# Kernel tuning notes

Hardware: AMD Instinct MI355X
Metric: run time of the kernel (lower is better)

Reference implementation:

```python
import jax, jax.numpy as jnp
import numpy as np

B, D, E = 8192, 4096, 64
TOP_K = 2
NOISE_EPSILON = 0.01


def setup_inputs() -> dict:
    key = jax.random.key(0)
    k1, k2, k3, k4 = jax.random.split(key, 4)
    return {
        "x": jax.random.normal(k1, (B, D), dtype=jnp.float32),
        # nn.Linear weights, init std=0.1, no bias; torch stores [out, in]
        "gate_w": jax.random.normal(k2, (E, D), dtype=jnp.float32) * 0.1,
        "noise_gate_w": jax.random.normal(k3, (E, D), dtype=jnp.float32) * 0.1,
        # deterministic stand-in for torch.randn_like(clean_logits)
        "noise": jax.random.normal(k4, (B, E), dtype=jnp.float32),
    }


def reference(x, gate_w, noise_gate_w, noise):
    # clean_logits = x @ W_g^T : [B, E]
    clean_logits = jnp.einsum("bd,ed->be", x, gate_w)
    # training path: noisy logits with softplus-scaled noise
    noise_logits = jnp.einsum("bd,ed->be", x, noise_gate_w)
    noisy_logits = clean_logits + noise * jax.nn.softplus(noise_logits) * NOISE_EPSILON
    # top-k over experts, softmax over the k selected logits
    top_k_logits, top_k_indices = jax.lax.top_k(noisy_logits, TOP_K)  # [B, k]
    top_k_gates = jax.nn.softmax(top_k_logits, axis=-1)
    # scatter back into dense [B, E] gates
    rows = jnp.arange(noisy_logits.shape[0])[:, None]  # [B, 1]
    gates = jnp.zeros_like(noisy_logits).at[rows, top_k_indices].set(top_k_gates)
    load = jax.nn.softmax(clean_logits, axis=-1)
    return (gates, load)
```

## Files before the change

### kernel.cpp

```cpp
#include <hip/hip_runtime.h>
#include <math.h>

#define BB 8192
#define DD 4096
#define EE 64

constexpr float NOISE_EPS = 0.01f;
constexpr int BM  = 64;
constexpr int BK  = 32;
constexpr int WRN = 128;

typedef __attribute__((ext_vector_type(8))) _Float16 f16x8;
typedef __attribute__((ext_vector_type(4))) float    f32x4;

__device__ __forceinline__ void split8(const float4& a, const float4& b,
                                       f16x8& hi, f16x8& mi) {
    float v[8] = {a.x, a.y, a.z, a.w, b.x, b.y, b.z, b.w};
    #pragma unroll
    for (int j = 0; j < 8; ++j) {
        _Float16 h = (_Float16)v[j];
        hi[j] = h;
        mi[j] = (_Float16)(v[j] - (float)h);
    }
}

__device__ __forceinline__ void gl_lds16(const void* g, void* l) {
    __builtin_amdgcn_global_load_lds(
        (const __attribute__((address_space(1))) unsigned*)g,
        (__attribute__((address_space(3))) unsigned*)l, 16, 0, 0);
}

__global__ __launch_bounds__(256) void wsplit_pack(
    const float* __restrict__ gw, const float* __restrict__ ngw,
    char* __restrict__ wpk)
{
    const int gid = blockIdx.x * 256 + threadIdx.x;
    const int r   = gid >> 9;
    const int kc  = gid & 511;
    const int k0  = kc * 8;
    const float* src = (r < EE) ? gw + (size_t)r * DD + k0
                                : ngw + (size_t)(r - EE) * DD + k0;
    float4 a = *reinterpret_cast<const float4*>(src);
    float4 b = *reinterpret_cast<const float4*>(src + 4);
    f16x8 hi, mi;
    split8(a, b, hi, mi);
    const int T    = k0 >> 5;
    const int kq   = (k0 >> 3) & 3;
    const int cb   = r >> 4;
    const int lane = kq * 16 + (r & 15);
    char* base = wpk + (size_t)T * 16384;
    *reinterpret_cast<f16x8*>(base + ((cb * 2 + 0) * 64 + lane) * 16) = hi;
    *reinterpret_cast<f16x8*>(base + ((cb * 2 + 1) * 64 + lane) * 16) = mi;
}

template <int SK>
__global__ __launch_bounds__(512, 4) void gating_main(
    const float* __restrict__ x,
    const char*  __restrict__ wpk,
    float* __restrict__ partial)
{
    constexpr int KC  = DD / SK;
    constexpr int NKS = KC / BK;

    __shared__ __align__(1024) char xbuf[2][8192];
    __shared__ __align__(1024) char wbuf[2][16384];

    const int tid  = threadIdx.x;
    const int bid  = blockIdx.x;
    const int sk   = bid & (SK - 1);
    const int row0 = (bid / SK) * BM;
    const int lane = tid & 63;
    const int wv   = tid >> 6;
    const int wmi  = wv >> 2;
    const int wni  = wv & 3;
    const int l15  = lane & 15;
    const int kq   = lane >> 4;

    const int xrow = tid >> 3;
    const int xch  = tid & 7;
    const float* xg = x + (size_t)(row0 + xrow) * DD + sk * KC
                        + ((xch ^ (xrow & 7)) << 2);
    const char* wg = wpk + (size_t)(sk * NKS) * 16384 + tid * 16;

    char* xd0 = xbuf[0] + wv * 1024;  char* xd1 = xbuf[1] + wv * 1024;
    char* wa0 = wbuf[0] + wv * 1024;  char* wa1 = wbuf[1] + wv * 1024;
    char* wb0 = wbuf[0] + 8192 + wv * 1024;  char* wb1 = wbuf[1] + 8192 + wv * 1024;

    int xoff[2][2];
    #pragma unroll
    for (int mb = 0; mb < 2; ++mb) {
        const int r = wmi * 32 + mb * 16 + l15;
        #pragma unroll
        for (int u = 0; u < 2; ++u)
            xoff[mb][u] = r * 128 + (((kq * 2 + u) ^ (r & 7)) << 4);
    }
    int boff[2][2];
    #pragma unroll
    for (int nb = 0; nb < 2; ++nb) {
        const int cb = wni * 2 + nb;
        #pragma unroll
        for (int p = 0; p < 2; ++p)
            boff[nb][p] = ((cb * 2 + p) * 64 + lane) * 16;
    }

    f32x4 acc00 = {0.f,0.f,0.f,0.f}, acc01 = {0.f,0.f,0.f,0.f};
    f32x4 acc10 = {0.f,0.f,0.f,0.f}, acc11 = {0.f,0.f,0.f,0.f};

    gl_lds16(xg,            xd0);
    gl_lds16(wg,            wa0);
    gl_lds16(wg + 8192,     wb0);
    gl_lds16(xg + BK,       xd1);
    gl_lds16(wg + 16384,    wa1);
    gl_lds16(wg + 16384 + 8192, wb1);
    asm volatile("s_waitcnt vmcnt(3)" ::: "memory");
    __builtin_amdgcn_s_barrier();

    #pragma unroll 2
    for (int t = 0; t < NKS; ++t) {
        const int c = t & 1;
        const char* xb = xbuf[c];
        const char* wb = wbuf[c];

        f16x8 ah0, am0, ah1, am1;
        {
            float4 a0 = *reinterpret_cast<const float4*>(xb + xoff[0][0]);
            float4 a1 = *reinterpret_cast<const float4*>(xb + xoff[0][1]);
            float4 a2 = *reinterpret_cast<const float4*>(xb + xoff[1][0]);
            float4 a3 = *reinterpret_cast<const float4*>(xb + xoff[1][1]);
            split8(a0, a1, ah0, am0);
            split8(a2, a3, ah1, am1);
        }
        f16x8 bh0 = *reinterpret_cast<const f16x8*>(wb + boff[0][0]);
        f16x8 bm0 = *reinterpret_cast<const f16x8*>(wb + boff[0][1]);
        f16x8 bh1 = *reinterpret_cast<const f16x8*>(wb + boff[1][0]);
        f16x8 bm1 = *reinterpret_cast<const f16x8*>(wb + boff[1][1]);

        acc00 = __builtin_amdgcn_mfma_f32_16x16x32_f16(ah0, bh0, acc00, 0, 0, 0);
        acc01 = __builtin_amdgcn_mfma_f32_16x16x32_f16(ah0, bh1, acc01, 0, 0, 0);
        acc10 = __builtin_amdgcn_mfma_f32_16x16x32_f16(ah1, bh0, acc10, 0, 0, 0);
        acc11 = __builtin_amdgcn_mfma_f32_16x16x32_f16(ah1, bh1, acc11, 0, 0, 0);
        acc00 = __builtin_amdgcn_mfma_f32_16x16x32_f16(am0, bh0, acc00, 0, 0, 0);
        acc01 = __builtin_amdgcn_mfma_f32_16x16x32_f16(am0, bh1, acc01, 0, 0, 0);
        acc10 = __builtin_amdgcn_mfma_f32_16x16x32_f16(am1, bh0, acc10, 0, 0, 0);
        acc11 = __builtin_amdgcn_mfma_f32_16x16x32_f16(am1, bh1, acc11, 0, 0, 0);
        acc00 = __builtin_amdgcn_mfma_f32_16x16x32_f16(ah0, bm0, acc00, 0, 0, 0);
        acc01 = __builtin_amdgcn_mfma_f32_16x16x32_f16(ah0, bm1, acc01, 0, 0, 0);
        acc10 = __builtin_amdgcn_mfma_f32_16x16x32_f16(ah1, bm0, acc10, 0, 0, 0);
        acc11 = __builtin_amdgcn_mfma_f32_16x16x32_f16(ah1, bm1, acc11, 0, 0, 0);

        asm volatile("s_waitcnt lgkmcnt(0)" ::: "memory");
        __builtin_amdgcn_s_barrier();

        if (t + 2 < NKS) {
            const char* wsrc = wg + (size_t)(t + 2) * 16384;
            gl_lds16(xg + (size_t)(t + 2) * BK, c ? xd1 : xd0);
            gl_lds16(wsrc,        c ? wa1 : wa0);
            gl_lds16(wsrc + 8192, c ? wb1 : wb0);
            asm volatile("s_waitcnt vmcnt(3)" ::: "memory");
        } else {
            asm volatile("s_waitcnt vmcnt(0)" ::: "memory");
        }
        __builtin_amdgcn_s_barrier();
    }

    const size_t pbase = ((size_t)sk * BB + row0) * 128;
    #pragma unroll
    for (int j = 0; j < 4; ++j) {
        const int r0 = wmi * 32 + kq * 4 + j;
        const int c0 = wni * 32 + l15;
        partial[pbase + (size_t)r0 * 128 + c0]           = acc00[j];
        partial[pbase + (size_t)r0 * 128 + c0 + 16]      = acc01[j];
        partial[pbase + (size_t)(r0 + 16) * 128 + c0]      = acc10[j];
        partial[pbase + (size_t)(r0 + 16) * 128 + c0 + 16] = acc11[j];
    }
}

template <int SK>
__global__ __launch_bounds__(512) void gating_epi(
    const float* __restrict__ partial,
    const float* __restrict__ noise,
    float* __restrict__ out)
{
    const int tid  = threadIdx.x;
    const int wv   = tid >> 6;
    const int lane = tid & 63;
    const int l15  = lane & 15;
    const int kq   = lane >> 4;
    const int grow = blockIdx.x * 32 + wv * 4 + kq;
    const int s    = l15;

    const float* pb = partial + (size_t)grow * 128 + 4 * s;
    float4 c4 = {0.f,0.f,0.f,0.f}, n4 = {0.f,0.f,0.f,0.f};
    #pragma unroll
    for (int k = 0; k < SK; ++k) {
        const float* p = pb + (size_t)k * BB * 128;
        float4 a = *reinterpret_cast<const float4*>(p);
        float4 b = *reinterpret_cast<const float4*>(p + 64);
        c4.x += a.x; c4.y += a.y; c4.z += a.z; c4.w += a.w;
        n4.x += b.x; n4.y += b.y; n4.z += b.z; n4.w += b.w;
    }

    float4 nz = *reinterpret_cast<const float4*>(noise + (size_t)grow * EE + 4 * s);

    float cc[4] = {c4.x, c4.y, c4.z, c4.w};
    float nl[4] = {n4.x, n4.y, n4.z, n4.w};
    float m1 = -3.4e38f, m2 = -3.4e38f;
    int   i1 = -1, i2 = -1;
    float cmax = -3.4e38f;
    #pragma unroll
    for (int j = 0; j < 4; ++j) {
        const int e = 4 * s + j;
        float sp  = fmaxf(nl[j], 0.0f) + log1pf(expf(-fabsf(nl[j])));
        float nzj = (j == 0) ? nz.x : (j == 1) ? nz.y : (j == 2) ? nz.z : nz.w;
        float vno = fmaf(nzj * sp, NOISE_EPS, cc[j]);
        if (vno > m1)      { m2 = m1; i2 = i1; m1 = vno; i1 = e; }
        else if (vno > m2) { m2 = vno; i2 = e; }
        cmax = fmaxf(cmax, cc[j]);
    }

    #pragma unroll
    for (int m = 1; m < 16; m <<= 1) {
        float b1 = __shfl_xor(m1, m, 16);
        int  bi1 = __shfl_xor(i1, m, 16);
        float b2 = __shfl_xor(m2, m, 16);
        int  bi2 = __shfl_xor(i2, m, 16);
        cmax = fmaxf(cmax, __shfl_xor(cmax, m, 16));

        bool bwin = (b1 > m1) || (b1 == m1 && bi1 < i1);
        float t1; int ti1; float t2; int ti2;
        if (bwin) {
            t1 = b1; ti1 = bi1;
            bool aw = (m1 > b2) || (m1 == b2 && i1 < bi2);
            t2 = aw ? m1 : b2; ti2 = aw ? i1 : bi2;
        } else {
            t1 = m1; ti1 = i1;
            bool bw = (b1 > m2) || (b1 == m2 && bi1 < i2);
            t2 = bw ? b1 : m2; ti2 = bw ? bi1 : i2;
        }
        m1 = t1; i1 = ti1; m2 = t2; i2 = ti2;
    }

    float tq = expf(m2 - m1);
    float p1 = 1.0f / (1.0f + tq);
    float p2 = tq * p1;

    float e0 = expf(cc[0] - cmax);
    float e1 = expf(cc[1] - cmax);
    float e2 = expf(cc[2] - cmax);
    float e3 = expf(cc[3] - cmax);
    float sum = e0 + e1 + e2 + e3;
    #pragma unroll
    for (int m = 1; m < 16; m <<= 1) sum += __shfl_xor(sum, m, 16);
    float inv = 1.0f / sum;

    const int eb = 4 * s;
    float4 gt;
    gt.x = (eb     == i1) ? p1 : (eb     == i2) ? p2 : 0.0f;
    gt.y = (eb + 1 == i1) ? p1 : (eb + 1 == i2) ? p2 : 0.0f;
    gt.z = (eb + 2 == i1) ? p1 : (eb + 2 == i2) ? p2 : 0.0f;
    gt.w = (eb + 3 == i1) ? p1 : (eb + 3 == i2) ? p2 : 0.0f;
    float4 ld = {e0 * inv, e1 * inv, e2 * inv, e3 * inv};

    *reinterpret_cast<float4*>(out + (size_t)grow * EE + eb) = gt;
    *reinterpret_cast<float4*>(out + (size_t)BB * EE + (size_t)grow * EE + eb) = ld;
}

extern "C" void kernel_launch(void* const* d_in, const int* in_sizes, int n_in,
                              void* d_out, int out_size, void* d_ws, size_t ws_size,
                              hipStream_t stream) {
    const float* x     = (const float*)d_in[0];
    const float* gw    = (const float*)d_in[1];
    const float* ngw   = (const float*)d_in[2];
    const float* noise = (const float*)d_in[3];
    float* out = (float*)d_out;

    char*  wpk     = (char*)d_ws;
    float* partial = (float*)(wpk + (size_t)2 * 1024 * 1024);

    const size_t MB = 1024 * 1024;

    hipLaunchKernelGGL(wsplit_pack, dim3(256), dim3(256), 0, stream, gw, ngw, wpk);

    if (ws_size >= 18 * MB) {
        hipLaunchKernelGGL(gating_main<4>, dim3((BB / BM) * 4), dim3(512), 0, stream,
                           x, wpk, partial);
        hipLaunchKernelGGL(gating_epi<4>, dim3(BB / 32), dim3(512), 0, stream,
                           partial, noise, out);
    } else if (ws_size >= 10 * MB) {
        hipLaunchKernelGGL(gating_main<2>, dim3((BB / BM) * 2), dim3(512), 0, stream,
                           x, wpk, partial);
        hipLaunchKernelGGL(gating_epi<2>, dim3(BB / 32), dim3(512), 0, stream,
                           partial, noise, out);
    } else {
        hipLaunchKernelGGL(gating_main<1>, dim3(BB / BM), dim3(512), 0, stream,
                           x, wpk, partial);
        hipLaunchKernelGGL(gating_epi<1>, dim3(BB / 32), dim3(512), 0, stream,
                           partial, noise, out);
    }
}
```

Baseline: 54.81 us.

## Deepen x prefetch to three stages and remap warps to 16x64 tiles

The main GEMM kernel now triple-buffers the x tiles while keeping double-buffered weights, so x loads are issued three steps ahead and weight loads two steps ahead. Warps are remapped from a 2x4 grid of 32x32 tiles to a 4x2 grid of 16x64 tiles. Each warp now splits only one 16-row A fragment per step, which cuts the redundant fp32-to-fp16 hi/lo split work, but it issues more B-fragment LDS reads. The loop always issues loads, clamping the index on the last steps, which adds a few redundant loads and uses more shared memory.

Result: faster. 52.17 us (-4.8%).

```diff
diff --git a/kernel.cpp b/kernel.cpp
--- a/kernel.cpp
+++ b/kernel.cpp
@@ -8,7 +8,6 @@
 constexpr float NOISE_EPS = 0.01f;
 constexpr int BM  = 64;
 constexpr int BK  = 32;
-constexpr int WRN = 128;
 
 typedef __attribute__((ext_vector_type(8))) _Float16 f16x8;
 typedef __attribute__((ext_vector_type(4))) float    f32x4;
@@ -62,7 +61,7 @@
     constexpr int KC  = DD / SK;
     constexpr int NKS = KC / BK;
 
-    __shared__ __align__(1024) char xbuf[2][8192];
+    __shared__ __align__(1024) char xbuf[3][8192];
     __shared__ __align__(1024) char wbuf[2][16384];
 
     const int tid  = threadIdx.x;
@@ -71,8 +70,8 @@
     const int row0 = (bid / SK) * BM;
     const int lane = tid & 63;
     const int wv   = tid >> 6;
-    const int wmi  = wv >> 2;
-    const int wni  = wv & 3;
+    const int wmi  = wv >> 1;
+    const int wni  = wv & 1;
     const int l15  = lane & 15;
     const int kq   = lane >> 4;
 
@@ -82,96 +81,80 @@
                         + ((xch ^ (xrow & 7)) << 2);
     const char* wg = wpk + (size_t)(sk * NKS) * 16384 + tid * 16;
 
-    char* xd0 = xbuf[0] + wv * 1024;  char* xd1 = xbuf[1] + wv * 1024;
-    char* wa0 = wbuf[0] + wv * 1024;  char* wa1 = wbuf[1] + wv * 1024;
-    char* wb0 = wbuf[0] + 8192 + wv * 1024;  char* wb1 = wbuf[1] + 8192 + wv * 1024;
-
-    int xoff[2][2];
-    #pragma unroll
-    for (int mb = 0; mb < 2; ++mb) {
-        const int r = wmi * 32 + mb * 16 + l15;
+    const int ldst = wv * 1024;
+
+    const int ar = wmi * 16 + l15;
+    const int xoff0 = ar * 128 + (((kq * 2 + 0) ^ (ar & 7)) << 4);
+    const int xoff1 = ar * 128 + (((kq * 2 + 1) ^ (ar & 7)) << 4);
+    int boff[4][2];
+    #pragma unroll
+    for (int nb = 0; nb < 4; ++nb) {
+        const int cb = wni * 4 + nb;
+        boff[nb][0] = ((cb * 2 + 0) * 64 + lane) * 16;
+        boff[nb][1] = ((cb * 2 + 1) * 64 + lane) * 16;
+    }
+
+    f32x4 acc[4];
+    #pragma unroll
+    for (int nb = 0; nb < 4; ++nb) acc[nb] = {0.f, 0.f, 0.f, 0.f};
+
+    char* xc  = (char*)xbuf[0];
+    char* xn1 = (char*)xbuf[1];
+    char* xn2 = (char*)xbuf[2];
+    char* wc  = (char*)wbuf[0];
+    char* wn  = (char*)wbuf[1];
+
+    gl_lds16(wg,                wc + ldst);
+    gl_lds16(wg + 8192,         wc + 8192 + ldst);
+    gl_lds16(xg,                xc + ldst);
+    gl_lds16(wg + 16384,        wn + ldst);
+    gl_lds16(wg + 16384 + 8192, wn + 8192 + ldst);
+    gl_lds16(xg + BK,           xn1 + ldst);
+    gl_lds16(xg + 2 * BK,       xn2 + ldst);
+    asm volatile("s_waitcnt vmcnt(4)" ::: "memory");
+    __builtin_amdgcn_s_barrier();
+
+    for (int t = 0; t < NKS; ++t) {
+        f16x8 ah, am;
+        {
+            float4 a0 = *reinterpret_cast<const float4*>(xc + xoff0);
+            float4 a1 = *reinterpret_cast<const float4*>(xc + xoff1);
+            split8(a0, a1, ah, am);
+        }
         #pragma unroll
-        for (int u = 0; u < 2; ++u)
-            xoff[mb][u] = r * 128 + (((kq * 2 + u) ^ (r & 7)) << 4);
-    }
-    int boff[2][2];
-    #pragma unroll
-    for (int nb = 0; nb < 2; ++nb) {
-        const int cb = wni * 2 + nb;
-        #pragma unroll
-        for (int p = 0; p < 2; ++p)
-            boff[nb][p] = ((cb * 2 + p) * 64 + lane) * 16;
-    }
-
-    f32x4 acc00 = {0.f,0.f,0.f,0.f}, acc01 = {0.f,0.f,0.f,0.f};
-    f32x4 acc10 = {0.f,0.f,0.f,0.f}, acc11 = {0.f,0.f,0.f,0.f};
-
-    gl_lds16(xg,            xd0);
-    gl_lds16(wg,            wa0);
-    gl_lds16(wg + 8192,     wb0);
-    gl_lds16(xg + BK,       xd1);
-    gl_lds16(wg + 16384,    wa1);
-    gl_lds16(wg + 16384 + 8192, wb1);
-    asm volatile("s_waitcnt vmcnt(3)" ::: "memory");
-    __builtin_amdgcn_s_barrier();
-
-    #pragma unroll 2
-    for (int t = 0; t < NKS; ++t) {
-        const int c = t & 1;
-        const char* xb = xbuf[c];
-        const char* wb = wbuf[c];
-
-        f16x8 ah0, am0, ah1, am1;
-        {
-            float4 a0 = *reinterpret_cast<const float4*>(xb + xoff[0][0]);
-            float4 a1 = *reinterpret_cast<const float4*>(xb + xoff[0][1]);
-            float4 a2 = *reinterpret_cast<const float4*>(xb + xoff[1][0]);
-            float4 a3 = *reinterpret_cast<const float4*>(xb + xoff[1][1]);
-            split8(a0, a1, ah0, am0);
-            split8(a2, a3, ah1, am1);
-        }
-        f16x8 bh0 = *reinterpret_cast<const f16x8*>(wb + boff[0][0]);
-        f16x8 bm0 = *reinterpret_cast<const f16x8*>(wb + boff[0][1]);
-        f16x8 bh1 = *reinterpret_cast<const f16x8*>(wb + boff[1][0]);
-        f16x8 bm1 = *reinterpret_cast<const f16x8*>(wb + boff[1][1]);
-
-        acc00 = __builtin_amdgcn_mfma_f32_16x16x32_f16(ah0, bh0, acc00, 0, 0, 0);
-        acc01 = __builtin_amdgcn_mfma_f32_16x16x32_f16(ah0, bh1, acc01, 0, 0, 0);
-        acc10 = __builtin_amdgcn_mfma_f32_16x16x32_f16(ah1, bh0, acc10, 0, 0, 0);
-        acc11 = __builtin_amdgcn_mfma_f32_16x16x32_f16(ah1, bh1, acc11, 0, 0, 0);
-        acc00 = __builtin_amdgcn_mfma_f32_16x16x32_f16(am0, bh0, acc00, 0, 0, 0);
-        acc01 = __builtin_amdgcn_mfma_f32_16x16x32_f16(am0, bh1, acc01, 0, 0, 0);
-        acc10 = __builtin_amdgcn_mfma_f32_16x16x32_f16(am1, bh0, acc10, 0, 0, 0);
-        acc11 = __builtin_amdgcn_mfma_f32_16x16x32_f16(am1, bh1, acc11, 0, 0, 0);
-        acc00 = __builtin_amdgcn_mfma_f32_16x16x32_f16(ah0, bm0, acc00, 0, 0, 0);
-        acc01 = __builtin_amdgcn_mfma_f32_16x16x32_f16(ah0, bm1, acc01, 0, 0, 0);
-        acc10 = __builtin_amdgcn_mfma_f32_16x16x32_f16(ah1, bm0, acc10, 0, 0, 0);
-        acc11 = __builtin_amdgcn_mfma_f32_16x16x32_f16(ah1, bm1, acc11, 0, 0, 0);
+        for (int nb = 0; nb < 4; ++nb) {
+            f16x8 bh = *reinterpret_cast<const f16x8*>(wc + boff[nb][0]);
+            f16x8 bm = *reinterpret_cast<const f16x8*>(wc + boff[nb][1]);
+            acc[nb] = __builtin_amdgcn_mfma_f32_16x16x32_f16(ah, bh, acc[nb], 0, 0, 0);
+            acc[nb] = __builtin_amdgcn_mfma_f32_16x16x32_f16(am, bh, acc[nb], 0, 0, 0);
+            acc[nb] = __builtin_amdgcn_mfma_f32_16x16x32_f16(ah, bm, acc[nb], 0, 0, 0);
+        }
 
         asm volatile("s_waitcnt lgkmcnt(0)" ::: "memory");
         __builtin_amdgcn_s_barrier();
 
-        if (t + 2 < NKS) {
-            const char* wsrc = wg + (size_t)(t + 2) * 16384;
-            gl_lds16(xg + (size_t)(t + 2) * BK, c ? xd1 : xd0);
-            gl_lds16(wsrc,        c ? wa1 : wa0);
-            gl_lds16(wsrc + 8192, c ? wb1 : wb0);
-            asm volatile("s_waitcnt vmcnt(3)" ::: "memory");
-        } else {
-            asm volatile("s_waitcnt vmcnt(0)" ::: "memory");
-        }
+        const int tw = (t + 2 < NKS) ? (t + 2) : (NKS - 1);
+        const int tx = (t + 3 < NKS) ? (t + 3) : (NKS - 1);
+        gl_lds16(wg + (size_t)tw * 16384,        wc + ldst);
+        gl_lds16(wg + (size_t)tw * 16384 + 8192, wc + 8192 + ldst);
+        gl_lds16(xg + (size_t)tx * BK,           xc + ldst);
+        asm volatile("s_waitcnt vmcnt(4)" ::: "memory");
         __builtin_amdgcn_s_barrier();
-    }
+
+        char* xt = xc; xc = xn1; xn1 = xn2; xn2 = xt;
+        char* wt = wc; wc = wn;  wn  = wt;
+    }
+    asm volatile("s_waitcnt vmcnt(0)" ::: "memory");
 
     const size_t pbase = ((size_t)sk * BB + row0) * 128;
     #pragma unroll
-    for (int j = 0; j < 4; ++j) {
-        const int r0 = wmi * 32 + kq * 4 + j;
-        const int c0 = wni * 32 + l15;
-        partial[pbase + (size_t)r0 * 128 + c0]           = acc00[j];
-        partial[pbase + (size_t)r0 * 128 + c0 + 16]      = acc01[j];
-        partial[pbase + (size_t)(r0 + 16) * 128 + c0]      = acc10[j];
-        partial[pbase + (size_t)(r0 + 16) * 128 + c0 + 16] = acc11[j];
+    for (int nb = 0; nb < 4; ++nb) {
+        #pragma unroll
+        for (int j = 0; j < 4; ++j) {
+            const int r = wmi * 16 + kq * 4 + j;
+            const int c = wni * 64 + nb * 16 + l15;
+            partial[pbase + (size_t)r * 128 + c] = acc[nb][j];
+        }
     }
 }
 
```
